# Optimization experiments

Hardware: AMD Instinct MI355X
Metric: run time of the kernel (lower is better)

Reference implementation:

```python
import jax, jax.numpy as jnp
import numpy as np

N_NODES = 100000
N_EDGES = 1000000
DIM_IN = 64
DIM_H = 64
DIM_OUT = 1


def _lin_init(key, out_dim, in_dim):
    # torch Linear default: U(-1/sqrt(fan_in), 1/sqrt(fan_in))
    bound = 1.0 / np.sqrt(in_dim)
    return jax.random.uniform(key, (out_dim, in_dim), jnp.float32, -bound, bound)


def setup_inputs() -> dict:
    key = jax.random.key(0)
    ks = jax.random.split(key, 10)
    x = jax.random.normal(ks[0], (N_NODES, DIM_IN), jnp.float32)
    edge_index = jax.random.randint(ks[1], (2, N_EDGES), 0, N_NODES, dtype=jnp.int64)
    # layer 0: SAGEConv(DIM_IN, DIM_H): lin_l (with bias) on aggregated neighbors, lin_r (no bias) on root
    Wl0 = _lin_init(ks[2], DIM_H, DIM_IN)
    bl0 = jax.random.uniform(ks[3], (DIM_H,), jnp.float32, -1.0 / np.sqrt(DIM_IN), 1.0 / np.sqrt(DIM_IN))
    Wr0 = _lin_init(ks[4], DIM_H, DIM_IN)
    # layer 1: SAGEConv(DIM_H, DIM_OUT)
    Wl1 = _lin_init(ks[5], DIM_OUT, DIM_H)
    bl1 = jax.random.uniform(ks[6], (DIM_OUT,), jnp.float32, -1.0 / np.sqrt(DIM_H), 1.0 / np.sqrt(DIM_H))
    Wr1 = _lin_init(ks[7], DIM_OUT, DIM_H)
    return {"x": x, "edge_index": edge_index,
            "Wl0": Wl0, "bl0": bl0, "Wr0": Wr0,
            "Wl1": Wl1, "bl1": bl1, "Wr1": Wr1}


def sage_conv(h, src, dst, Wl, bl, Wr):
    # messages: gather source-node features per edge, mean-aggregate into destination nodes
    msg = h[src]                                                   # [E, d]
    summed = jax.ops.segment_sum(msg, dst, num_segments=N_NODES)   # [N, d]
    deg = jax.ops.segment_sum(jnp.ones((src.shape[0],), h.dtype), dst, num_segments=N_NODES)
    mean_nb = summed / jnp.maximum(deg, 1.0)[:, None]
    # out = lin_l(mean_neighbors) + lin_r(x_root)
    return mean_nb @ Wl.T + bl + h @ Wr.T


def reference(x, edge_index, Wl0, bl0, Wr0, Wl1, bl1, Wr1):
    src, dst = edge_index[0], edge_index[1]
    h = sage_conv(x, src, dst, Wl0, bl0, Wr0)
    h = jax.nn.relu(h)  # dropout is identity in eval mode
    h = sage_conv(h, src, dst, Wl1, bl1, Wr1)
    return (h, jax.nn.sigmoid(h))
```

## Files before the change

### kernel.cpp

```cpp
#include <hip/hip_runtime.h>
#include <hip/hip_bf16.h>
#include <math.h>

#define N_NODES 100000
#define N_EDGES 1000000
#define DIM 64
#define SCAN_BLOCKS 391
#define AGPAD 72
#define NCOPY 8

typedef __hip_bfloat16 bf16;
typedef __attribute__((ext_vector_type(8))) short short8;
typedef __attribute__((ext_vector_type(4))) float floatx4;

__device__ __forceinline__ float b2f(bf16 v) { return __bfloat162float(v); }

__device__ __forceinline__ unsigned int packbf2(float a, float b) {
    bf16 x = __float2bfloat16(a), y = __float2bfloat16(b);
    unsigned short ux = *(unsigned short*)&x, uy = *(unsigned short*)&y;
    return (unsigned int)ux | ((unsigned int)uy << 16);
}

__device__ __forceinline__ short f2bs(float v) {
    bf16 x = __float2bfloat16(v);
    return *(short*)&x;
}

__device__ __forceinline__ float2 upk(unsigned int u) {
    unsigned short lo = (unsigned short)(u & 0xffff);
    unsigned short hi = (unsigned short)(u >> 16);
    bf16 a = *(bf16*)&lo, b = *(bf16*)&hi;
    return make_float2(b2f(a), b2f(b));
}

__device__ __forceinline__ int clampN(int v) {
    return v < 0 ? 0 : (v >= N_NODES ? N_NODES - 1 : v);
}

__global__ void hist_convert_kernel(const int* __restrict__ ei,
                                    int* __restrict__ degi8,
                                    int* __restrict__ pos,
                                    const float4* __restrict__ x4,
                                    uint2* __restrict__ xb4,
                                    const float* __restrict__ Wl0,
                                    const float* __restrict__ Wr0,
                                    short* __restrict__ wt) {
    int b = blockIdx.x;
    if (b < 977) {
        int idx = b * 256 + threadIdx.x;
        if (idx < N_EDGES / 4) {
            int* dg = degi8 + (b & (NCOPY - 1)) * N_NODES;
            int4 d4 = ((const int4*)(ei + N_EDGES))[idx];
            int4 p;
            p.x = atomicAdd(&dg[clampN(d4.x)], 1);
            p.y = atomicAdd(&dg[clampN(d4.y)], 1);
            p.z = atomicAdd(&dg[clampN(d4.z)], 1);
            p.w = atomicAdd(&dg[clampN(d4.w)], 1);
            ((int4*)pos)[idx] = p;
        }
    } else if (b < 7227) {
        int idx = (b - 977) * 256 + threadIdx.x;
        float4 f = x4[idx];
        xb4[idx] = make_uint2(packbf2(f.x, f.y), packbf2(f.z, f.w));
    } else {
        for (int i = threadIdx.x; i < 8192; i += 256) {
            int d = i >> 7, k = i & 127;
            float v = (k < 64) ? Wl0[d * 64 + k] : Wr0[d * 64 + (k - 64)];
            wt[i] = f2bs(v);
        }
    }
}

__global__ void scan1_kernel(int* __restrict__ degi8,
                             int* __restrict__ degi,
                             int* __restrict__ rowstart, int* __restrict__ bsum) {
    __shared__ int sc[256];
    int t = threadIdx.x;
    int i = blockIdx.x * 256 + t;
    int v = 0;
    if (i < N_NODES) {
        int sum = 0;
        #pragma unroll
        for (int c = 0; c < NCOPY; ++c) {
            int u = degi8[c * N_NODES + i];
            degi8[c * N_NODES + i] = sum;
            sum += u;
        }
        degi[i] = sum;
        v = sum;
    }
    sc[t] = v;
    __syncthreads();
    #pragma unroll
    for (int off = 1; off < 256; off <<= 1) {
        int u = (t >= off) ? sc[t - off] : 0;
        __syncthreads();
        sc[t] += u;
        __syncthreads();
    }
    if (i < N_NODES) rowstart[i] = sc[t] - v;
    if (t == 255) bsum[blockIdx.x] = sc[t];
}

__global__ void scan2_kernel(int* __restrict__ bsum) {
    __shared__ int sc[512];
    int t = threadIdx.x;
    int v = (t < SCAN_BLOCKS) ? bsum[t] : 0;
    sc[t] = v;
    __syncthreads();
    #pragma unroll
    for (int off = 1; off < 512; off <<= 1) {
        int u = (t >= off) ? sc[t - off] : 0;
        __syncthreads();
        sc[t] += u;
        __syncthreads();
    }
    if (t < SCAN_BLOCKS) bsum[t] = sc[t] - v;
}

__global__ void fill_kernel(const int* __restrict__ ei,
                            const int* __restrict__ rowstart,
                            const int* __restrict__ bsum,
                            const int* __restrict__ degi8,
                            const int* __restrict__ pos,
                            int* __restrict__ csr) {
    int idx = blockIdx.x * blockDim.x + threadIdx.x;
    if (idx < N_EDGES / 4) {
        const int* dg = degi8 + ((idx >> 8) & (NCOPY - 1)) * N_NODES;
        int4 s4 = ((const int4*)ei)[idx];
        int4 d4 = ((const int4*)(ei + N_EDGES))[idx];
        int4 p4 = ((const int4*)pos)[idx];
        int d;
        d = clampN(d4.x); csr[rowstart[d] + bsum[d >> 8] + dg[d] + p4.x] = clampN(s4.x);
        d = clampN(d4.y); csr[rowstart[d] + bsum[d >> 8] + dg[d] + p4.y] = clampN(s4.y);
        d = clampN(d4.z); csr[rowstart[d] + bsum[d >> 8] + dg[d] + p4.z] = clampN(s4.z);
        d = clampN(d4.w); csr[rowstart[d] + bsum[d >> 8] + dg[d] + p4.w] = clampN(s4.w);
    }
}

__global__ __launch_bounds__(256) void agg_gemm_kernel(
        const uint2* __restrict__ xb2, const short* __restrict__ xb,
        const short* __restrict__ wt,
        const int* __restrict__ rowstart, const int* __restrict__ bsum,
        const int* __restrict__ degi, const int* __restrict__ csr,
        const float* __restrict__ bl0, const float* __restrict__ Wl1,
        const float* __restrict__ Wr1,
        float* __restrict__ s, float* __restrict__ t) {
    __shared__ short As[16 * AGPAD];
    __shared__ float sRed[16], tRed[16];
    const int tid = threadIdx.x;
    const int nb = blockIdx.x * 16;

    if (tid < 16) { sRed[tid] = 0.0f; tRed[tid] = 0.0f; }

    {
        int qn = tid >> 4;
        int l  = tid & 15;
        int n = nb + qn;
        int beg = rowstart[n] + bsum[n >> 8];
        int cnt = degi[n];
        float4 A0 = make_float4(0.f, 0.f, 0.f, 0.f);
        float4 A1 = A0, A2 = A0, A3 = A0;
        int i = 0;
        for (; i + 4 <= cnt; i += 4) {
            int e0 = csr[beg + i],     e1 = csr[beg + i + 1];
            int e2 = csr[beg + i + 2], e3 = csr[beg + i + 3];
            uint2 u0 = xb2[(long)e0 * 16 + l];
            uint2 u1 = xb2[(long)e1 * 16 + l];
            uint2 u2 = xb2[(long)e2 * 16 + l];
            uint2 u3 = xb2[(long)e3 * 16 + l];
            float2 f; 
            f = upk(u0.x); A0.x += f.x; A0.y += f.y; f = upk(u0.y); A0.z += f.x; A0.w += f.y;
            f = upk(u1.x); A1.x += f.x; A1.y += f.y; f = upk(u1.y); A1.z += f.x; A1.w += f.y;
            f = upk(u2.x); A2.x += f.x; A2.y += f.y; f = upk(u2.y); A2.z += f.x; A2.w += f.y;
            f = upk(u3.x); A3.x += f.x; A3.y += f.y; f = upk(u3.y); A3.z += f.x; A3.w += f.y;
        }
        if (i < cnt) {
            uint2 u = xb2[(long)csr[beg + i] * 16 + l];
            float2 f = upk(u.x); A0.x += f.x; A0.y += f.y;
            f = upk(u.y); A0.z += f.x; A0.w += f.y;
        }
        if (i + 1 < cnt) {
            uint2 u = xb2[(long)csr[beg + i + 1] * 16 + l];
            float2 f = upk(u.x); A1.x += f.x; A1.y += f.y;
            f = upk(u.y); A1.z += f.x; A1.w += f.y;
        }
        if (i + 2 < cnt) {
            uint2 u = xb2[(long)csr[beg + i + 2] * 16 + l];
            float2 f = upk(u.x); A2.x += f.x; A2.y += f.y;
            f = upk(u.y); A2.z += f.x; A2.w += f.y;
        }
        float inv = 1.0f / fmaxf((float)cnt, 1.0f);
        float ax = (A0.x + A1.x + A2.x + A3.x) * inv;
        float ay = (A0.y + A1.y + A2.y + A3.y) * inv;
        float az = (A0.z + A1.z + A2.z + A3.z) * inv;
        float aw = (A0.w + A1.w + A2.w + A3.w) * inv;
        *(uint2*)&As[qn * AGPAD + 4 * l] =
            make_uint2(packbf2(ax, ay), packbf2(az, aw));
    }
    __syncthreads();

    const int lane = tid & 63;
    const int w = tid >> 6;
    const int r = lane & 15;
    const int quad = lane >> 4;

    short8 a0 = *(const short8*)&As[r * AGPAD + quad * 8];
    short8 a1 = *(const short8*)&As[r * AGPAD + 32 + quad * 8];
    const long xrow = (long)(nb + r) * 64 + quad * 8;
    short8 a2 = *(const short8*)(xb + xrow);
    short8 a3 = *(const short8*)(xb + xrow + 32);

    const int d = w * 16 + r;
    const short* brow = wt + (long)d * 128 + quad * 8;
    short8 b0 = *(const short8*)(brow);
    short8 b1 = *(const short8*)(brow + 32);
    short8 b2 = *(const short8*)(brow + 64);
    short8 b3 = *(const short8*)(brow + 96);

    float bb = bl0[d];
    floatx4 acc = {bb, bb, bb, bb};
    acc = __builtin_amdgcn_mfma_f32_16x16x32_bf16(a0, b0, acc, 0, 0, 0);
    acc = __builtin_amdgcn_mfma_f32_16x16x32_bf16(a1, b1, acc, 0, 0, 0);
    acc = __builtin_amdgcn_mfma_f32_16x16x32_bf16(a2, b2, acc, 0, 0, 0);
    acc = __builtin_amdgcn_mfma_f32_16x16x32_bf16(a3, b3, acc, 0, 0, 0);

    float w1 = Wl1[d], w2 = Wr1[d];
    float hs[4], ht[4];
    #pragma unroll
    for (int g = 0; g < 4; ++g) {
        float h = fmaxf(acc[g], 0.0f);
        hs[g] = h * w1;
        ht[g] = h * w2;
    }
    #pragma unroll
    for (int g = 0; g < 4; ++g) {
        #pragma unroll
        for (int off = 1; off < 16; off <<= 1) {
            hs[g] += __shfl_xor(hs[g], off, 64);
            ht[g] += __shfl_xor(ht[g], off, 64);
        }
    }
    if (r == 0) {
        #pragma unroll
        for (int g = 0; g < 4; ++g) {
            atomicAdd(&sRed[quad * 4 + g], hs[g]);
            atomicAdd(&tRed[quad * 4 + g], ht[g]);
        }
    }
    __syncthreads();
    if (tid < 16) {
        s[nb + tid] = sRed[tid];
        t[nb + tid] = tRed[tid];
    }
}

__global__ void final_kernel(const float* __restrict__ s,
                             const float* __restrict__ t,
                             const int* __restrict__ rowstart,
                             const int* __restrict__ bsum,
                             const int* __restrict__ degi,
                             const int* __restrict__ csr,
                             const float* __restrict__ bl1,
                             float* __restrict__ out) {
    int n = blockIdx.x * 256 + threadIdx.x;
    if (n >= N_NODES) return;
    int beg = rowstart[n] + bsum[n >> 8];
    int cnt = degi[n];
    float acc = 0.0f;
    int i = 0;
    for (; i + 4 <= cnt; i += 4) {
        int e0 = csr[beg + i], e1 = csr[beg + i + 1];
        int e2 = csr[beg + i + 2], e3 = csr[beg + i + 3];
        acc += s[e0] + s[e1] + s[e2] + s[e3];
    }
    for (; i < cnt; ++i) acc += s[csr[beg + i]];
    float v = acc / fmaxf((float)cnt, 1.0f) + bl1[0] + t[n];
    float sg = 1.0f / (1.0f + expf(-v));
    out[n] = v;
    out[N_NODES + n] = sg;
}

extern "C" void kernel_launch(void* const* d_in, const int* in_sizes, int n_in,
                              void* d_out, int out_size, void* d_ws, size_t ws_size,
                              hipStream_t stream) {
    const float* x   = (const float*)d_in[0];
    const int*   ei  = (const int*)d_in[1];
    const float* Wl0 = (const float*)d_in[2];
    const float* bl0 = (const float*)d_in[3];
    const float* Wr0 = (const float*)d_in[4];
    const float* Wl1 = (const float*)d_in[5];
    const float* bl1 = (const float*)d_in[6];
    const float* Wr1 = (const float*)d_in[7];
    float* out = (float*)d_out;

    char* ws = (char*)d_ws;
    int*   degi     = (int*)(ws);
    int*   rowstart = (int*)(ws + 400000);
    int*   bsum     = (int*)(ws + 800000);
    float* s        = (float*)(ws + 804096);
    float* t        = (float*)(ws + 1204096);
    int*   csr      = (int*)(ws + 1604096);
    int*   pos      = (int*)(ws + 5604096);
    char*  xb       = (ws + 9604096);
    short* wt       = (short*)(ws + 22404096);
    int*   degi8    = (int*)(ws + 22420480);

    (void)hipMemsetAsync(degi8, 0, NCOPY * N_NODES * sizeof(int), stream);

    hist_convert_kernel<<<7228, 256, 0, stream>>>(ei, degi8, pos,
                                                  (const float4*)x, (uint2*)xb,
                                                  Wl0, Wr0, wt);
    scan1_kernel<<<SCAN_BLOCKS, 256, 0, stream>>>(degi8, degi, rowstart, bsum);
    scan2_kernel<<<1, 512, 0, stream>>>(bsum);
    fill_kernel<<<977, 256, 0, stream>>>(ei, rowstart, bsum, degi8, pos, csr);
    agg_gemm_kernel<<<6250, 256, 0, stream>>>((const uint2*)xb, (const short*)xb,
                                              wt, rowstart, bsum, degi, csr,
                                              bl0, Wl1, Wr1, s, t);
    final_kernel<<<SCAN_BLOCKS, 256, 0, stream>>>(s, t, rowstart, bsum, degi, csr,
                                                  bl1, out);
}
```

Baseline: 203.4 us.

## Build CSR with per-block shared-memory byte-packed histograms instead of global atomics

Replaces the global-atomic degree histogram (8 replicated copies plus a per-edge position array) with 64 blocks. Each block counts its slice of edges into byte-packed counters in shared memory and writes them out; the scan turns these into per-block offsets, and the fill kernel replays shared-memory atomics to get each edge's local slot. This removes global atomics, the memset and the pos array traffic. In exchange only 64 blocks run during count and fill, each needs about 100KB of LDS, and per-block counts must stay under 256 per node.

```diff
diff --git a/kernel.cpp b/kernel.cpp
--- a/kernel.cpp
+++ b/kernel.cpp
@@ -7,7 +7,9 @@
 #define DIM 64
 #define SCAN_BLOCKS 391
 #define AGPAD 72
-#define NCOPY 8
+#define NHB 64
+#define EPB (N_EDGES / NHB)
+#define HWORDS ((N_NODES + 3) / 4)
 
 typedef __hip_bfloat16 bf16;
 typedef __attribute__((ext_vector_type(8))) short short8;
@@ -37,29 +39,31 @@
     return v < 0 ? 0 : (v >= N_NODES ? N_NODES - 1 : v);
 }
 
-__global__ void hist_convert_kernel(const int* __restrict__ ei,
-                                    int* __restrict__ degi8,
-                                    int* __restrict__ pos,
-                                    const float4* __restrict__ x4,
-                                    uint2* __restrict__ xb4,
-                                    const float* __restrict__ Wl0,
-                                    const float* __restrict__ Wr0,
-                                    short* __restrict__ wt) {
+
+__global__ __launch_bounds__(256) void count_kernel(const int* __restrict__ ei,
+                                                    unsigned int* __restrict__ bh32) {
+    __shared__ unsigned int cnt[HWORDS];
+    const int t = threadIdx.x, b = blockIdx.x;
+    for (int w = t; w < HWORDS; w += 256) cnt[w] = 0u;
+    __syncthreads();
+    const int* dst = ei + N_EDGES + b * EPB;
+    for (int k = t; k < EPB; k += 256) {
+        int d = clampN(dst[k]);
+        atomicAdd(&cnt[d >> 2], 1u << (8 * (d & 3)));
+    }
+    __syncthreads();
+    unsigned int* out = bh32 + (long)b * HWORDS;
+    for (int w = t; w < HWORDS; w += 256) out[w] = cnt[w];
+}
+
+__global__ void convert_kernel(const float4* __restrict__ x4,
+                               uint2* __restrict__ xb4,
+                               const float* __restrict__ Wl0,
+                               const float* __restrict__ Wr0,
+                               short* __restrict__ wt) {
     int b = blockIdx.x;
-    if (b < 977) {
+    if (b < 6250) {
         int idx = b * 256 + threadIdx.x;
-        if (idx < N_EDGES / 4) {
-            int* dg = degi8 + (b & (NCOPY - 1)) * N_NODES;
-            int4 d4 = ((const int4*)(ei + N_EDGES))[idx];
-            int4 p;
-            p.x = atomicAdd(&dg[clampN(d4.x)], 1);
-            p.y = atomicAdd(&dg[clampN(d4.y)], 1);
-            p.z = atomicAdd(&dg[clampN(d4.z)], 1);
-            p.w = atomicAdd(&dg[clampN(d4.w)], 1);
-            ((int4*)pos)[idx] = p;
-        }
-    } else if (b < 7227) {
-        int idx = (b - 977) * 256 + threadIdx.x;
         float4 f = x4[idx];
         xb4[idx] = make_uint2(packbf2(f.x, f.y), packbf2(f.z, f.w));
     } else {
@@ -71,7 +75,7 @@
     }
 }
 
-__global__ void scan1_kernel(int* __restrict__ degi8,
+__global__ void scan1_kernel(unsigned char* __restrict__ bhb,
                              int* __restrict__ degi,
                              int* __restrict__ rowstart, int* __restrict__ bsum) {
     __shared__ int sc[256];
@@ -81,9 +85,10 @@
     if (i < N_NODES) {
         int sum = 0;
         #pragma unroll
-        for (int c = 0; c < NCOPY; ++c) {
-            int u = degi8[c * N_NODES + i];
-            degi8[c * N_NODES + i] = sum;
+        for (int c = 0; c < NHB; ++c) {
+            long off = (long)c * (HWORDS * 4) + i;
+            int u = bhb[off];
+            bhb[off] = (unsigned char)sum;
             sum += u;
         }
         degi[i] = sum;
@@ -99,7 +104,7 @@
         __syncthreads();
     }
     if (i < N_NODES) rowstart[i] = sc[t] - v;
-    if (t == 255) bsum[blockIdx.x] = sc[t];
+    if (t == 255) bsum[blockIdx.x] = sc[t] - v + ((i < N_NODES) ? v : 0);
 }
 
 __global__ void scan2_kernel(int* __restrict__ bsum) {
@@ -118,23 +123,24 @@
     if (t < SCAN_BLOCKS) bsum[t] = sc[t] - v;
 }
 
-__global__ void fill_kernel(const int* __restrict__ ei,
-                            const int* __restrict__ rowstart,
-                            const int* __restrict__ bsum,
-                            const int* __restrict__ degi8,
-                            const int* __restrict__ pos,
-                            int* __restrict__ csr) {
-    int idx = blockIdx.x * blockDim.x + threadIdx.x;
-    if (idx < N_EDGES / 4) {
-        const int* dg = degi8 + ((idx >> 8) & (NCOPY - 1)) * N_NODES;
-        int4 s4 = ((const int4*)ei)[idx];
-        int4 d4 = ((const int4*)(ei + N_EDGES))[idx];
-        int4 p4 = ((const int4*)pos)[idx];
-        int d;
-        d = clampN(d4.x); csr[rowstart[d] + bsum[d >> 8] + dg[d] + p4.x] = clampN(s4.x);
-        d = clampN(d4.y); csr[rowstart[d] + bsum[d >> 8] + dg[d] + p4.y] = clampN(s4.y);
-        d = clampN(d4.z); csr[rowstart[d] + bsum[d >> 8] + dg[d] + p4.z] = clampN(s4.z);
-        d = clampN(d4.w); csr[rowstart[d] + bsum[d >> 8] + dg[d] + p4.w] = clampN(s4.w);
+__global__ __launch_bounds__(256) void fill_kernel(const int* __restrict__ ei,
+                                                   const int* __restrict__ rowstart,
+                                                   const int* __restrict__ bsum,
+                                                   const unsigned int* __restrict__ bh32,
+                                                   int* __restrict__ csr) {
+    __shared__ unsigned int cnt[HWORDS];
+    const int t = threadIdx.x, b = blockIdx.x;
+    const unsigned int* in = bh32 + (long)b * HWORDS;
+    for (int w = t; w < HWORDS; w += 256) cnt[w] = in[w];
+    __syncthreads();
+    const int* srcp = ei + b * EPB;
+    const int* dstp = ei + N_EDGES + b * EPB;
+    for (int k = t; k < EPB; k += 256) {
+        int d = clampN(dstp[k]);
+        int sv = clampN(srcp[k]);
+        unsigned int old = atomicAdd(&cnt[d >> 2], 1u << (8 * (d & 3)));
+        int local = (int)((old >> (8 * (d & 3))) & 0xffu);
+        csr[rowstart[d] + bsum[d >> 8] + local] = sv;
     }
 }
 
@@ -301,19 +307,18 @@
     float* s        = (float*)(ws + 804096);
     float* t        = (float*)(ws + 1204096);
     int*   csr      = (int*)(ws + 1604096);
-    int*   pos      = (int*)(ws + 5604096);
-    char*  xb       = (ws + 9604096);
-    short* wt       = (short*)(ws + 22404096);
-    int*   degi8    = (int*)(ws + 22420480);
-
-    (void)hipMemsetAsync(degi8, 0, NCOPY * N_NODES * sizeof(int), stream);
-
-    hist_convert_kernel<<<7228, 256, 0, stream>>>(ei, degi8, pos,
-                                                  (const float4*)x, (uint2*)xb,
-                                                  Wl0, Wr0, wt);
-    scan1_kernel<<<SCAN_BLOCKS, 256, 0, stream>>>(degi8, degi, rowstart, bsum);
+    char*  xb       = (ws + 5604096);
+    short* wt       = (short*)(ws + 18404096);
+    char*  bh       = (ws + 18420480);
+
+    count_kernel<<<NHB, 256, 0, stream>>>(ei, (unsigned int*)bh);
+    convert_kernel<<<6251, 256, 0, stream>>>((const float4*)x, (uint2*)xb,
+                                             Wl0, Wr0, wt);
+    scan1_kernel<<<SCAN_BLOCKS, 256, 0, stream>>>((unsigned char*)bh, degi,
+                                                  rowstart, bsum);
     scan2_kernel<<<1, 512, 0, stream>>>(bsum);
-    fill_kernel<<<977, 256, 0, stream>>>(ei, rowstart, bsum, degi8, pos, csr);
+    fill_kernel<<<NHB, 256, 0, stream>>>(ei, rowstart, bsum,
+                                         (const unsigned int*)bh, csr);
     agg_gemm_kernel<<<6250, 256, 0, stream>>>((const uint2*)xb, (const short*)xb,
                                               wt, rowstart, bsum, degi, csr,
                                               bl0, Wl1, Wr1, s, t);
```

New measurement: 214.1 us. +5.3%, slower.
